# Kernel tuning notes

Measured on AMD Instinct MI355X. Metric: run time of the kernel, lower is better.

Reference implementation:

```python
import jax, jax.numpy as jnp
import numpy as np

N = 8192          # total nodes (bipartite: first half left, second half right)
E = 65536         # raw edges
D = 256           # emb_dim
H = 8             # heads
HD = D // H       # head_dim = 32
EAD = 2           # edge_attr_dim


def _init(k, shape, fan_in):
    return (jax.random.normal(k, shape, jnp.float32) / np.sqrt(fan_in)).astype(jnp.float32)


def setup_inputs() -> dict:
    key = jax.random.key(0)
    ks = jax.random.split(key, 16)
    x = jax.random.normal(ks[0], (N, D), jnp.float32)
    src = jax.random.randint(ks[1], (E,), 0, N // 2, jnp.int32)
    dst = jax.random.randint(ks[2], (E,), N // 2, N, jnp.int32)
    edge_index = jnp.stack([src, dst])                       # [2, E]
    edge_attr = jax.random.uniform(ks[3], (E, EAD), jnp.float32)
    query_mask = jax.random.randint(ks[4], (E,), 0, 2, jnp.int32).astype(bool)
    return {
        "x": x,
        "edge_index": edge_index,
        "edge_attr": edge_attr,
        "query_mask": query_mask,
        "start_right": N // 2,
        "W_kqv": _init(ks[5], (D, 3 * D), D), "b_kqv": jnp.zeros((3 * D,), jnp.float32),
        "W_edge": _init(ks[6], (EAD, D), EAD), "b_edge": jnp.zeros((D,), jnp.float32),
        "W_att1": _init(ks[7], (3 * HD, HD), 3 * HD), "b_att1": jnp.zeros((HD,), jnp.float32),
        "W_att2": _init(ks[8], (HD, 1), HD), "b_att2": jnp.zeros((1,), jnp.float32),
        "W_out": _init(ks[9], (D, D), D), "b_out": jnp.zeros((D,), jnp.float32),
        "bn_gamma": jnp.ones((D,), jnp.float32), "bn_beta": jnp.zeros((D,), jnp.float32),
    }


def _build_graph(edge_index, query_mask, n):
    """Replicates MetaGNN.forward edge preprocessing (static, int-only)."""
    ei = np.asarray(edge_index)
    qm = np.asarray(query_mask).astype(bool)
    sup = np.where(~qm)[0]                                   # support edges
    # cat([edge_index[:, support], edge_index.flip(0)], dim=1)
    src = np.concatenate([ei[0, sup], ei[1]])
    dst = np.concatenate([ei[1, sup], ei[0]])
    attr_idx = np.concatenate([sup, np.arange(ei.shape[1])])
    # remove_self_loops
    keep = src != dst
    src, dst, attr_idx = src[keep], dst[keep], attr_idx[keep]
    # add_self_loops with fill_value [0, 0]
    loops = np.arange(n)
    src = np.concatenate([src, loops])
    dst = np.concatenate([dst, loops])
    return jnp.asarray(src), jnp.asarray(dst), jnp.asarray(attr_idx)


def _layer(x, src, dst, ea, W_kqv, b_kqv, W_edge, b_edge, W_att1, b_att1,
           W_att2, b_att2, W_out, b_out, bn_gamma, bn_beta):
    n = x.shape[0]
    kqv = x @ W_kqv + b_kqv                                  # [N, 3D]
    q = kqv[dst, :D].reshape(-1, H, HD)                      # x_i (target)
    k = kqv[src, D:2 * D].reshape(-1, H, HD) / np.sqrt(HD)   # x_j (source)
    v = kqv[src, 2 * D:].reshape(-1, H, HD)
    ef = jax.nn.relu((ea @ W_edge + b_edge).reshape(-1, H, HD))
    feat = jnp.concatenate([k, q, ef], axis=-1)              # [E, H, 3*HD]
    hdn = jax.nn.relu(jnp.einsum('ehf,fd->ehd', feat, W_att1) + b_att1)
    logits = (jnp.einsum('ehd,do->eho', hdn, W_att2) + b_att2)[..., 0]  # [E, H]
    # scatter-softmax over destination node segments
    m = jax.ops.segment_max(logits, dst, num_segments=n)
    a = jnp.exp(logits - m[dst])
    s = jax.ops.segment_sum(a, dst, num_segments=n)
    alpha = a / (s[dst] + 1e-16)                             # [E, H]
    msg = (alpha[..., None] * v).reshape(-1, D) @ W_out + b_out
    out = jax.ops.segment_sum(msg, dst, num_segments=n) + x  # aggr='add' + residual
    # BatchNorm1d (training-mode batch statistics, eps=1e-5)
    mu = out.mean(axis=0)
    var = out.var(axis=0)
    return (out - mu) / jnp.sqrt(var + 1e-5) * bn_gamma + bn_beta


def reference(x, edge_index, edge_attr, query_mask, start_right,
              W_kqv, b_kqv, W_edge, b_edge, W_att1, b_att1, W_att2, b_att2,
              W_out, b_out, bn_gamma, bn_beta):
    n = x.shape[0]
    src, dst, attr_idx = _build_graph(edge_index, query_mask, n)
    ea = jnp.concatenate(
        [edge_attr[attr_idx], jnp.zeros((n, edge_attr.shape[1]), edge_attr.dtype)], axis=0)
    return _layer(x, src, dst, ea, W_kqv, b_kqv, W_edge, b_edge,
                  W_att1, b_att1, W_att2, b_att2, W_out, b_out, bn_gamma, bn_beta)
```

## Files before the change

### kernel.cpp

```cpp
#include <hip/hip_runtime.h>

#define N_NODES 8192
#define E_RAW   65536
#define NSLOT   (2*E_RAW + N_NODES)
#define DEGCAP  48
#define L_ITER  4

typedef __attribute__((ext_vector_type(8)))  short bf16x8;
typedef __attribute__((ext_vector_type(4)))  short bf16x4;
typedef __attribute__((ext_vector_type(4)))  float f32x4;
typedef __attribute__((ext_vector_type(16))) float f32x16;
typedef unsigned short u16;

__device__ __forceinline__ u16 f2b(float f) {
  unsigned u = __float_as_uint(f);
  u = (u + 0x7FFFu + ((u >> 16) & 1u)) >> 16;
  return (u16)u;
}
__device__ __forceinline__ float b2f(u16 b) {
  return __uint_as_float(((unsigned)b) << 16);
}

__global__ __launch_bounds__(256) void setup_k(
    const float* __restrict__ x, u16* __restrict__ xb,
    const float* __restrict__ W_kqv, const float* __restrict__ b_kqv,
    const float* __restrict__ W_att1, const float* __restrict__ b_att1,
    const float* __restrict__ W_edge, const float* __restrict__ b_edge,
    const float* __restrict__ W_out,
    u16* __restrict__ BcatT, float* __restrict__ biascat,
    u16* __restrict__ wa1t, u16* __restrict__ WoutT, float* __restrict__ beW,
    const int* __restrict__ ei, const int* __restrict__ qm,
    int* __restrict__ cnt, int* __restrict__ csr)
{
  __shared__ float tile[64][65];
  const float inv_sqrt_hd = 0.17677669529663687f;
  int bx = blockIdx.x, t = threadIdx.x;

  if (bx < 2048) {
    int i = bx * 256 + t;
    float4 v = ((const float4*)x)[i];
    ushort4 o;
    o.x = f2b(v.x); o.y = f2b(v.y); o.z = f2b(v.z); o.w = f2b(v.w);
    ((ushort4*)xb)[i] = o;
    return;
  }
  if (bx < 2836) {
    int c = bx - 2048;
    int i = t;
    if (c < 768) {
      float v;
      if (c < 256) {
        int h = c >> 5, d2 = c & 31;
        float s = 0.f;
        #pragma unroll
        for (int j = 0; j < 32; ++j)
          s += W_kqv[i*768 + 256 + h*32 + j] * W_att1[j*32 + d2];
        v = s * inv_sqrt_hd;
      } else if (c < 512) {
        int c2 = c - 256; int h = c2 >> 5, d2 = c2 & 31;
        float s = 0.f;
        #pragma unroll
        for (int j = 0; j < 32; ++j)
          s += W_kqv[i*768 + h*32 + j] * W_att1[(32+j)*32 + d2];
        v = s;
      } else {
        v = W_kqv[i*768 + c];
      }
      BcatT[(size_t)c * 256 + i] = f2b(v);
      if (i == 0) {
        float bv;
        if (c < 256) {
          int h = c >> 5, d2 = c & 31;
          float s = 0.f;
          for (int j = 0; j < 32; ++j)
            s += b_kqv[256 + h*32 + j] * W_att1[j*32 + d2];
          bv = s * inv_sqrt_hd;
        } else if (c < 512) {
          int c2 = c - 256; int h = c2 >> 5, d2 = c2 & 31;
          float s = 0.f;
          for (int j = 0; j < 32; ++j)
            s += b_kqv[h*32 + j] * W_att1[(32+j)*32 + d2];
          bv = s + b_att1[c2 & 31];
        } else {
          bv = b_kqv[c];
        }
        biascat[c] = bv;
      }
    } else if (c < 772) {
      int idx = (c - 768) * 256 + i;
      int d2 = idx >> 5, j = idx & 31;
      wa1t[idx] = f2b(W_att1[(64 + j) * 32 + d2]);
    } else {
      int b = c - 772;
      int r0 = (b >> 2) * 64, c0 = (b & 3) * 64;
      for (int idx = i; idx < 4096; idx += 256) {
        int r = idx >> 6, cc = idx & 63;
        tile[r][cc] = W_out[(size_t)(r0 + r) * 256 + c0 + cc];
      }
      __syncthreads();
      for (int idx = i; idx < 4096; idx += 256) {
        int cc = idx >> 6, r = idx & 63;
        WoutT[(size_t)(c0 + cc) * 256 + r0 + r] = f2b(tile[r][cc]);
      }
    }
    return;
  }
  if (bx == 2836) {
    int h = t >> 5, d2 = t & 31;
    float s = 0.f;
    #pragma unroll
    for (int f = 0; f < 32; ++f)
      s += fmaxf(b_edge[h*32 + f], 0.f) * W_att1[(64 + f)*32 + d2];
    beW[h*32 + d2] = s;
    return;
  }
  int slot = (bx - 2837) * 256 + t;
  if (slot >= NSLOT) return;
  int src, dst;
  if (slot < E_RAW) {
    if (qm[slot] != 0) return;
    src = ei[slot]; dst = ei[E_RAW + slot];
  } else if (slot < 2*E_RAW) {
    int e = slot - E_RAW;
    src = ei[E_RAW + e]; dst = ei[e];
  } else {
    int n = slot - 2*E_RAW;
    src = n; dst = n;
  }
  int pos = atomicAdd(&cnt[dst], 1);
  if (pos < DEGCAP) csr[dst*DEGCAP + pos] = (slot << 13) | src;
}

__global__ __launch_bounds__(256) void gemm_nf_k(const u16* __restrict__ xb,
                                                 const u16* __restrict__ BcatT,
                                                 const float* __restrict__ biascat,
                                                 u16* __restrict__ nodeF) {
  int t = threadIdx.x, lane = t & 63, wid = t >> 6;
  int r0 = (blockIdx.y * 4 + wid) * 32;
  int c0 = blockIdx.x * 32;
  int lr = lane & 15, lk = (lane >> 4) * 8;
  f32x4 acc00 = {0.f,0.f,0.f,0.f}, acc01 = {0.f,0.f,0.f,0.f};
  f32x4 acc10 = {0.f,0.f,0.f,0.f}, acc11 = {0.f,0.f,0.f,0.f};
  for (int k0 = 0; k0 < 256; k0 += 32) {
    bf16x8 a0 = *(const bf16x8*)&xb[(size_t)(r0 + lr) * 256 + k0 + lk];
    bf16x8 a1 = *(const bf16x8*)&xb[(size_t)(r0 + 16 + lr) * 256 + k0 + lk];
    bf16x8 b0 = *(const bf16x8*)&BcatT[(size_t)(c0 + lr) * 256 + k0 + lk];
    bf16x8 b1 = *(const bf16x8*)&BcatT[(size_t)(c0 + 16 + lr) * 256 + k0 + lk];
    acc00 = __builtin_amdgcn_mfma_f32_16x16x32_bf16(a0, b0, acc00, 0, 0, 0);
    acc01 = __builtin_amdgcn_mfma_f32_16x16x32_bf16(a0, b1, acc01, 0, 0, 0);
    acc10 = __builtin_amdgcn_mfma_f32_16x16x32_bf16(a1, b0, acc10, 0, 0, 0);
    acc11 = __builtin_amdgcn_mfma_f32_16x16x32_bf16(a1, b1, acc11, 0, 0, 0);
  }
  float bias0 = biascat[c0 + lr];
  float bias1 = biascat[c0 + 16 + lr];
  int rbase = r0 + (lane >> 4) * 4;
  #pragma unroll
  for (int r = 0; r < 4; ++r) {
    nodeF[(size_t)(rbase + r) * 768 + c0 + lr]           = f2b(acc00[r] + bias0);
    nodeF[(size_t)(rbase + r) * 768 + c0 + 16 + lr]      = f2b(acc01[r] + bias1);
    nodeF[(size_t)(rbase + 16 + r) * 768 + c0 + lr]      = f2b(acc10[r] + bias0);
    nodeF[(size_t)(rbase + 16 + r) * 768 + c0 + 16 + lr] = f2b(acc11[r] + bias1);
  }
}

__global__ __launch_bounds__(256) void logits_k(
    const int* __restrict__ ei, const int* __restrict__ qm,
    const float* __restrict__ eattr, const u16* __restrict__ nf,
    const u16* __restrict__ wa1t,
    const float* __restrict__ W_edge, const float* __restrict__ b_edge,
    const float* __restrict__ W_att2, const float* __restrict__ beW,
    float* __restrict__ lgd)
{
  __shared__ __align__(16) u16 kqls[4][16][8][40];

  int bx = blockIdx.x, t = threadIdx.x, lane = t & 63, wid = t >> 6;
  int col = lane & 31;
  int e = col >> 3, h = col & 7, hi = lane >> 5;

  float w2r[16];
  #pragma unroll
  for (int r = 0; r < 16; ++r)
    w2r[r] = W_att2[(r & 3) + 8*(r >> 2) + 4*hi];

  if (bx < 1024) {
    float ce0[16], ce1[16], cbe[16];
    #pragma unroll
    for (int i = 0; i < 8; ++i) {
      int fA = hi*8 + i, fB = 16 + hi*8 + i;
      ce0[i]   = W_edge[h*32 + fA];       ce0[8+i] = W_edge[h*32 + fB];
      ce1[i]   = W_edge[256 + h*32 + fA]; ce1[8+i] = W_edge[256 + h*32 + fB];
      cbe[i]   = b_edge[h*32 + fA];       cbe[8+i] = b_edge[h*32 + fB];
    }
    bf16x8 af0 = *(const bf16x8*)&wa1t[(lane & 31)*32 + hi*8];
    bf16x8 af1 = *(const bf16x8*)&wa1t[(lane & 31)*32 + 16 + hi*8];

    for (int it = 0; it < L_ITER; ++it) {
      int er0 = ((bx * L_ITER + it) * 4 + wid) * 4;
      int er = er0 + e;
      int eqm = qm[er];
      float2 ea = *(const float2*)&eattr[2*er];

      #pragma unroll
      for (int m = 0; m < 8; ++m) {
        int flat = m*64 + lane;
        int ri = flat >> 5, chunk = flat & 31;
        int ee = ri & 3, ty = ri >> 2;
        int erow = er0 + ee;
        int node = (ty & 1) ? ei[E_RAW + erow] : ei[erow];
        int koff = (ty >> 1) ? 256 : 0;
        bf16x8 v = *(const bf16x8*)&nf[(size_t)node*768 + koff + chunk*8];
        *(bf16x8*)&kqls[wid][ri][chunk >> 2][(chunk & 3)*8] = v;
      }

      bf16x8 bf0, bf1;
      #pragma unroll
      for (int i = 0; i < 8; ++i) {
        float v0 = fmaf(ea.x, ce0[i],   fmaf(ea.y, ce1[i],   cbe[i]));
        float v1 = fmaf(ea.x, ce0[8+i], fmaf(ea.y, ce1[8+i], cbe[8+i]));
        bf0[i] = (short)f2b(fmaxf(v0, 0.f));
        bf1[i] = (short)f2b(fmaxf(v1, 0.f));
      }
      f32x16 acc = {};
      acc = __builtin_amdgcn_mfma_f32_32x32x16_bf16(af0, bf0, acc, 0, 0, 0);
      acc = __builtin_amdgcn_mfma_f32_32x32x16_bf16(af1, bf1, acc, 0, 0, 0);

      __builtin_amdgcn_wave_barrier();

      float lg0 = 0.f, lg1 = 0.f;
      #pragma unroll
      for (int q = 0; q < 4; ++q) {
        int off = q*8 + 4*hi;
        bf16x4 k0 = *(const bf16x4*)&kqls[wid][e][h][off];
        bf16x4 q0 = *(const bf16x4*)&kqls[wid][12 + e][h][off];
        bf16x4 k1 = *(const bf16x4*)&kqls[wid][4 + e][h][off];
        bf16x4 q1 = *(const bf16x4*)&kqls[wid][8 + e][h][off];
        #pragma unroll
        for (int j = 0; j < 4; ++j) {
          int r = q*4 + j;
          float efw = acc[r];
          float p0 = efw + b2f((u16)k0[j]) + b2f((u16)q0[j]);
          float p1 = efw + b2f((u16)k1[j]) + b2f((u16)q1[j]);
          lg0 = fmaf(fmaxf(p0, 0.f), w2r[r], lg0);
          lg1 = fmaf(fmaxf(p1, 0.f), w2r[r], lg1);
        }
      }
      lg0 += __shfl_xor(lg0, 32);
      lg1 += __shfl_xor(lg1, 32);
      if (hi == 0) {
        if (eqm == 0) lgd[(size_t)er*8 + h] = lg0;
        lgd[(size_t)(E_RAW + er)*8 + h] = lg1;
      }
      __builtin_amdgcn_wave_barrier();
    }
  } else {
    float bew[16];
    #pragma unroll
    for (int r = 0; r < 16; ++r)
      bew[r] = beW[h*32 + (r & 3) + 8*(r >> 2) + 4*hi];

    for (int it = 0; it < L_ITER; ++it) {
      int n0 = (((bx - 1024) * L_ITER + it) * 4 + wid) * 4;
      int nn = n0 + e;
      #pragma unroll
      for (int m = 0; m < 4; ++m) {
        int flat = m*64 + lane;
        int ri = flat >> 5, chunk = flat & 31;
        int ee = ri & 3, ty = ri >> 2;
        int node = n0 + ee;
        bf16x8 v = *(const bf16x8*)&nf[(size_t)node*768 + (ty ? 256 : 0) + chunk*8];
        *(bf16x8*)&kqls[wid][ri][chunk >> 2][(chunk & 3)*8] = v;
      }
      __builtin_amdgcn_wave_barrier();
      float lg0 = 0.f;
      #pragma unroll
      for (int q = 0; q < 4; ++q) {
        int off = q*8 + 4*hi;
        bf16x4 k0 = *(const bf16x4*)&kqls[wid][e][h][off];
        bf16x4 q0 = *(const bf16x4*)&kqls[wid][4 + e][h][off];
        #pragma unroll
        for (int j = 0; j < 4; ++j) {
          int r = q*4 + j;
          float p = bew[r] + b2f((u16)k0[j]) + b2f((u16)q0[j]);
          lg0 = fmaf(fmaxf(p, 0.f), w2r[r], lg0);
        }
      }
      lg0 += __shfl_xor(lg0, 32);
      if (hi == 0) lgd[(size_t)(2*E_RAW + nn)*8 + h] = lg0;
      __builtin_amdgcn_wave_barrier();
    }
  }
}

__global__ __launch_bounds__(256) void aggr_k(const int* __restrict__ cnt,
                                              const int* __restrict__ csr,
                                              const float* __restrict__ lgd,
                                              const u16* __restrict__ nf,
                                              u16* __restrict__ aggb) {
  int t = threadIdx.x, lane = t & 63, wid = t >> 6;
  int n = blockIdx.x * 4 + wid;
  int deg = cnt[n]; if (deg > DEGCAP) deg = DEGCAP;

  float m = -3.4e38f, s = 0.f;
  for (int i = lane >> 3; i < deg; i += 8) {
    int pk = csr[n*DEGCAP + i];
    float val = lgd[(size_t)((unsigned)pk >> 13)*8 + (lane & 7)];
    float mn = fmaxf(m, val);
    s = s * __expf(m - mn) + __expf(val - mn);
    m = mn;
  }
  #pragma unroll
  for (int msk = 8; msk <= 32; msk <<= 1) {
    float mo = __shfl_xor(m, msk), so = __shfl_xor(s, msk);
    float mn = fmaxf(m, mo);
    s = s * __expf(m - mn) + so * __expf(mo - mn);
    m = mn;
  }
  float sinv = 1.f / (s + 1e-16f);
  int head = lane >> 3;
  float mh = __shfl(m, head);
  float sh = __shfl(sinv, head);

  float ac0 = 0.f, ac1 = 0.f, ac2 = 0.f, ac3 = 0.f;
  const u16* vb = nf + 512 + lane * 4;
  #pragma unroll 2
  for (int i = 0; i < deg; ++i) {
    int pk = csr[n*DEGCAP + i];
    int slot = (unsigned)pk >> 13, srcv = pk & 8191;
    float a = __expf(lgd[(size_t)slot*8 + head] - mh) * sh;
    bf16x4 v = *(const bf16x4*)&vb[(size_t)srcv * 768];
    ac0 = fmaf(a, b2f((u16)v[0]), ac0);
    ac1 = fmaf(a, b2f((u16)v[1]), ac1);
    ac2 = fmaf(a, b2f((u16)v[2]), ac2);
    ac3 = fmaf(a, b2f((u16)v[3]), ac3);
  }
  ushort4 o; o.x = f2b(ac0); o.y = f2b(ac1); o.z = f2b(ac2); o.w = f2b(ac3);
  *(ushort4*)&aggb[(size_t)n * 256 + lane * 4] = o;
}

__global__ __launch_bounds__(256) void gemmout_k(const u16* __restrict__ aggb,
                                                 const u16* __restrict__ WoutT,
                                                 const float* __restrict__ x,
                                                 const int* __restrict__ cnt,
                                                 const float* __restrict__ b_out,
                                                 float* __restrict__ out,
                                                 float* __restrict__ bnsum,
                                                 float* __restrict__ bnsq) {
  int t = threadIdx.x, lane = t & 63, wid = t >> 6;
  int r0 = (blockIdx.y * 4 + wid) * 32;
  int c0 = blockIdx.x * 32;
  int lr = lane & 15, lk = (lane >> 4) * 8;
  f32x4 acc00 = {0.f,0.f,0.f,0.f}, acc01 = {0.f,0.f,0.f,0.f};
  f32x4 acc10 = {0.f,0.f,0.f,0.f}, acc11 = {0.f,0.f,0.f,0.f};
  for (int k0 = 0; k0 < 256; k0 += 32) {
    bf16x8 a0 = *(const bf16x8*)&aggb[(size_t)(r0 + lr) * 256 + k0 + lk];
    bf16x8 a1 = *(const bf16x8*)&aggb[(size_t)(r0 + 16 + lr) * 256 + k0 + lk];
    bf16x8 b0 = *(const bf16x8*)&WoutT[(size_t)(c0 + lr) * 256 + k0 + lk];
    bf16x8 b1 = *(const bf16x8*)&WoutT[(size_t)(c0 + 16 + lr) * 256 + k0 + lk];
    acc00 = __builtin_amdgcn_mfma_f32_16x16x32_bf16(a0, b0, acc00, 0, 0, 0);
    acc01 = __builtin_amdgcn_mfma_f32_16x16x32_bf16(a0, b1, acc01, 0, 0, 0);
    acc10 = __builtin_amdgcn_mfma_f32_16x16x32_bf16(a1, b0, acc10, 0, 0, 0);
    acc11 = __builtin_amdgcn_mfma_f32_16x16x32_bf16(a1, b1, acc11, 0, 0, 0);
  }
  int colA = c0 + lr, colB = c0 + 16 + lr;
  float bA = b_out[colA], bB = b_out[colB];
  int rbase = r0 + (lane >> 4) * 4;
  float sA = 0.f, qA = 0.f, sB = 0.f, qB = 0.f;
  #pragma unroll
  for (int r = 0; r < 4; ++r) {
    int rowA = rbase + r, rowB = rbase + 16 + r;
    float degA = (float)cnt[rowA], degB = (float)cnt[rowB];
    float v00 = acc00[r] + x[(size_t)rowA * 256 + colA] + degA * bA;
    float v01 = acc01[r] + x[(size_t)rowA * 256 + colB] + degA * bB;
    float v10 = acc10[r] + x[(size_t)rowB * 256 + colA] + degB * bA;
    float v11 = acc11[r] + x[(size_t)rowB * 256 + colB] + degB * bB;
    out[(size_t)rowA * 256 + colA] = v00;
    out[(size_t)rowA * 256 + colB] = v01;
    out[(size_t)rowB * 256 + colA] = v10;
    out[(size_t)rowB * 256 + colB] = v11;
    sA += v00 + v10; qA += v00*v00 + v10*v10;
    sB += v01 + v11; qB += v01*v01 + v11*v11;
  }
  #pragma unroll
  for (int msk = 16; msk <= 32; msk <<= 1) {
    sA += __shfl_xor(sA, msk); qA += __shfl_xor(qA, msk);
    sB += __shfl_xor(sB, msk); qB += __shfl_xor(qB, msk);
  }
  if (lane < 16) {
    atomicAdd(&bnsum[colA], sA); atomicAdd(&bnsq[colA], qA);
    atomicAdd(&bnsum[colB], sB); atomicAdd(&bnsq[colB], qB);
  }
}

__global__ __launch_bounds__(256) void bnapply_k(float* __restrict__ out,
                                                 const float* __restrict__ bnsum,
                                                 const float* __restrict__ bnsq,
                                                 const float* __restrict__ gamma,
                                                 const float* __restrict__ beta) {
  int t = threadIdx.x;
  int c4 = t & 63;
  int r = blockIdx.x * 4 + (t >> 6);
  float4 s4 = ((const float4*)bnsum)[c4];
  float4 q4 = ((const float4*)bnsq)[c4];
  float4 g4 = ((const float4*)gamma)[c4];
  float4 b4 = ((const float4*)beta)[c4];
  float4 v = ((const float4*)out)[(size_t)r * 64 + c4];
  #pragma unroll
  for (int j = 0; j < 4; ++j) {
    float mu = (&s4.x)[j] * (1.f / 8192.f);
    float var = (&q4.x)[j] * (1.f / 8192.f) - mu*mu;
    float inv = rsqrtf(var + 1e-5f);
    (&v.x)[j] = ((&v.x)[j] - mu) * inv * (&g4.x)[j] + (&b4.x)[j];
  }
  ((float4*)out)[(size_t)r * 64 + c4] = v;
}

extern "C" void kernel_launch(void* const* d_in, const int* in_sizes, int n_in,
                              void* d_out, int out_size, void* d_ws, size_t ws_size,
                              hipStream_t stream) {
  (void)in_sizes; (void)n_in; (void)out_size; (void)ws_size;
  const float* x      = (const float*)d_in[0];
  const int*   ei     = (const int*)d_in[1];
  const float* eattr  = (const float*)d_in[2];
  const int*   qm     = (const int*)d_in[3];
  const float* W_kqv  = (const float*)d_in[5];
  const float* b_kqv  = (const float*)d_in[6];
  const float* W_edge = (const float*)d_in[7];
  const float* b_edge = (const float*)d_in[8];
  const float* W_att1 = (const float*)d_in[9];
  const float* b_att1 = (const float*)d_in[10];
  const float* W_att2 = (const float*)d_in[11];
  const float* W_out  = (const float*)d_in[13];
  const float* b_out  = (const float*)d_in[14];
  const float* gamma  = (const float*)d_in[15];
  const float* beta   = (const float*)d_in[16];
  float* out = (float*)d_out;

  char* w = (char*)d_ws;
  u16*    xb      = (u16*)w;     w += (size_t)N_NODES*256*2;
  u16*    BcatT   = (u16*)w;     w += (size_t)768*256*2;
  u16*    wa1t    = (u16*)w;     w += 1024*2;
  u16*    WoutT   = (u16*)w;     w += (size_t)256*256*2;
  u16*    nodeFb  = (u16*)w;     w += (size_t)N_NODES*768*2;
  float*  biascat = (float*)w;   w += 768*4;
  float*  beW     = (float*)w;   w += 256*4;
  u16*    aggb    = (u16*)w;     w += (size_t)N_NODES*256*2;
  int*    cnt     = (int*)w;     w += N_NODES*4;
  float*  bnsum   = (float*)w;   w += 256*4;
  float*  bnsq    = (float*)w;   w += 256*4;
  int*    csr     = (int*)w;     w += (size_t)N_NODES*DEGCAP*4;
  float*  lgd     = (float*)w;   w += (size_t)NSLOT*8*4;

  hipMemsetAsync(cnt, 0, (size_t)(N_NODES + 512) * sizeof(int), stream);

  setup_k<<<2837 + (NSLOT + 255)/256, 256, 0, stream>>>(
      x, xb, W_kqv, b_kqv, W_att1, b_att1, W_edge, b_edge, W_out,
      BcatT, biascat, wa1t, WoutT, beW, ei, qm, cnt, csr);

  gemm_nf_k<<<dim3(768/32, N_NODES/128), 256, 0, stream>>>(xb, BcatT, biascat, nodeFb);

  logits_k<<<1024 + 128, 256, 0, stream>>>(ei, qm, eattr, nodeFb, wa1t,
                                           W_edge, b_edge, W_att2, beW, lgd);

  aggr_k<<<N_NODES/4, 256, 0, stream>>>(cnt, csr, lgd, nodeFb, aggb);

  gemmout_k<<<dim3(256/32, N_NODES/128), 256, 0, stream>>>(
      aggb, WoutT, x, cnt, b_out, out, bnsum, bnsq);

  bnapply_k<<<N_NODES/4, 256, 0, stream>>>(out, bnsum, bnsq, gamma, beta);
}
```

Baseline: 109.9 us.

## Replace memset with in-kernel zeroing and fuse CSR scatter into widened node GEMM

Removes the hipMemsetAsync by zeroing the counter/BN-sum region (2176 int4 = 8704 ints) inside setup_k's extra blocks. The edge-to-CSR scatter moves out of setup_k into the node-feature GEMM kernel, which now tiles 128x64 per block with 8 accumulators instead of 128x32. This cuts one launch and the memset, and lets the scatter atomics overlap the GEMM. The cost is higher register use in the GEMM blocks and a mixed-role grid.

```diff
diff --git a/kernel.cpp b/kernel.cpp
--- a/kernel.cpp
+++ b/kernel.cpp
@@ -29,8 +29,7 @@
     const float* __restrict__ W_out,
     u16* __restrict__ BcatT, float* __restrict__ biascat,
     u16* __restrict__ wa1t, u16* __restrict__ WoutT, float* __restrict__ beW,
-    const int* __restrict__ ei, const int* __restrict__ qm,
-    int* __restrict__ cnt, int* __restrict__ csr)
+    int4* __restrict__ zbase)
 {
   __shared__ float tile[64][65];
   const float inv_sqrt_hd = 0.17677669529663687f;
@@ -114,7 +113,53 @@
     beW[h*32 + d2] = s;
     return;
   }
-  int slot = (bx - 2837) * 256 + t;
+  int i = (bx - 2837) * 256 + t;
+  if (i < 2176) zbase[i] = make_int4(0, 0, 0, 0);
+}
+
+__global__ __launch_bounds__(256) void gemm_scatter_k(
+    const u16* __restrict__ xb, const u16* __restrict__ BcatT,
+    const float* __restrict__ biascat, u16* __restrict__ nodeF,
+    const int* __restrict__ ei, const int* __restrict__ qm,
+    int* __restrict__ cnt, int* __restrict__ csr)
+{
+  int bx = blockIdx.x, t = threadIdx.x;
+  if (bx < 768) {
+    int lane = t & 63, wid = t >> 6;
+    int cb = bx % 12, rb = bx / 12;
+    int r0 = rb * 128 + wid * 32;
+    int c0 = cb * 64;
+    int lr = lane & 15, lk = (lane >> 4) * 8;
+    f32x4 acc0[4] = {}, acc1[4] = {};
+    for (int k0 = 0; k0 < 256; k0 += 32) {
+      bf16x8 a0 = *(const bf16x8*)&xb[(size_t)(r0 + lr) * 256 + k0 + lk];
+      bf16x8 a1 = *(const bf16x8*)&xb[(size_t)(r0 + 16 + lr) * 256 + k0 + lk];
+      bf16x8 b0 = *(const bf16x8*)&BcatT[(size_t)(c0 + lr) * 256 + k0 + lk];
+      bf16x8 b1 = *(const bf16x8*)&BcatT[(size_t)(c0 + 16 + lr) * 256 + k0 + lk];
+      bf16x8 b2 = *(const bf16x8*)&BcatT[(size_t)(c0 + 32 + lr) * 256 + k0 + lk];
+      bf16x8 b3 = *(const bf16x8*)&BcatT[(size_t)(c0 + 48 + lr) * 256 + k0 + lk];
+      acc0[0] = __builtin_amdgcn_mfma_f32_16x16x32_bf16(a0, b0, acc0[0], 0, 0, 0);
+      acc0[1] = __builtin_amdgcn_mfma_f32_16x16x32_bf16(a0, b1, acc0[1], 0, 0, 0);
+      acc0[2] = __builtin_amdgcn_mfma_f32_16x16x32_bf16(a0, b2, acc0[2], 0, 0, 0);
+      acc0[3] = __builtin_amdgcn_mfma_f32_16x16x32_bf16(a0, b3, acc0[3], 0, 0, 0);
+      acc1[0] = __builtin_amdgcn_mfma_f32_16x16x32_bf16(a1, b0, acc1[0], 0, 0, 0);
+      acc1[1] = __builtin_amdgcn_mfma_f32_16x16x32_bf16(a1, b1, acc1[1], 0, 0, 0);
+      acc1[2] = __builtin_amdgcn_mfma_f32_16x16x32_bf16(a1, b2, acc1[2], 0, 0, 0);
+      acc1[3] = __builtin_amdgcn_mfma_f32_16x16x32_bf16(a1, b3, acc1[3], 0, 0, 0);
+    }
+    int rbase = r0 + (lane >> 4) * 4;
+    #pragma unroll
+    for (int cc = 0; cc < 4; ++cc) {
+      float bias = biascat[c0 + cc*16 + lr];
+      #pragma unroll
+      for (int r = 0; r < 4; ++r) {
+        nodeF[(size_t)(rbase + r) * 768 + c0 + cc*16 + lr]      = f2b(acc0[cc][r] + bias);
+        nodeF[(size_t)(rbase + 16 + r) * 768 + c0 + cc*16 + lr] = f2b(acc1[cc][r] + bias);
+      }
+    }
+    return;
+  }
+  int slot = (bx - 768) * 256 + t;
   if (slot >= NSLOT) return;
   int src, dst;
   if (slot < E_RAW) {
@@ -129,38 +174,6 @@
   }
   int pos = atomicAdd(&cnt[dst], 1);
   if (pos < DEGCAP) csr[dst*DEGCAP + pos] = (slot << 13) | src;
-}
-
-__global__ __launch_bounds__(256) void gemm_nf_k(const u16* __restrict__ xb,
-                                                 const u16* __restrict__ BcatT,
-                                                 const float* __restrict__ biascat,
-                                                 u16* __restrict__ nodeF) {
-  int t = threadIdx.x, lane = t & 63, wid = t >> 6;
-  int r0 = (blockIdx.y * 4 + wid) * 32;
-  int c0 = blockIdx.x * 32;
-  int lr = lane & 15, lk = (lane >> 4) * 8;
-  f32x4 acc00 = {0.f,0.f,0.f,0.f}, acc01 = {0.f,0.f,0.f,0.f};
-  f32x4 acc10 = {0.f,0.f,0.f,0.f}, acc11 = {0.f,0.f,0.f,0.f};
-  for (int k0 = 0; k0 < 256; k0 += 32) {
-    bf16x8 a0 = *(const bf16x8*)&xb[(size_t)(r0 + lr) * 256 + k0 + lk];
-    bf16x8 a1 = *(const bf16x8*)&xb[(size_t)(r0 + 16 + lr) * 256 + k0 + lk];
-    bf16x8 b0 = *(const bf16x8*)&BcatT[(size_t)(c0 + lr) * 256 + k0 + lk];
-    bf16x8 b1 = *(const bf16x8*)&BcatT[(size_t)(c0 + 16 + lr) * 256 + k0 + lk];
-    acc00 = __builtin_amdgcn_mfma_f32_16x16x32_bf16(a0, b0, acc00, 0, 0, 0);
-    acc01 = __builtin_amdgcn_mfma_f32_16x16x32_bf16(a0, b1, acc01, 0, 0, 0);
-    acc10 = __builtin_amdgcn_mfma_f32_16x16x32_bf16(a1, b0, acc10, 0, 0, 0);
-    acc11 = __builtin_amdgcn_mfma_f32_16x16x32_bf16(a1, b1, acc11, 0, 0, 0);
-  }
-  float bias0 = biascat[c0 + lr];
-  float bias1 = biascat[c0 + 16 + lr];
-  int rbase = r0 + (lane >> 4) * 4;
-  #pragma unroll
-  for (int r = 0; r < 4; ++r) {
-    nodeF[(size_t)(rbase + r) * 768 + c0 + lr]           = f2b(acc00[r] + bias0);
-    nodeF[(size_t)(rbase + r) * 768 + c0 + 16 + lr]      = f2b(acc01[r] + bias1);
-    nodeF[(size_t)(rbase + 16 + r) * 768 + c0 + lr]      = f2b(acc10[r] + bias0);
-    nodeF[(size_t)(rbase + 16 + r) * 768 + c0 + 16 + lr] = f2b(acc11[r] + bias1);
-  }
 }
 
 __global__ __launch_bounds__(256) void logits_k(
@@ -450,13 +463,12 @@
   int*    csr     = (int*)w;     w += (size_t)N_NODES*DEGCAP*4;
   float*  lgd     = (float*)w;   w += (size_t)NSLOT*8*4;
 
-  hipMemsetAsync(cnt, 0, (size_t)(N_NODES + 512) * sizeof(int), stream);
-
-  setup_k<<<2837 + (NSLOT + 255)/256, 256, 0, stream>>>(
+  setup_k<<<2846, 256, 0, stream>>>(
       x, xb, W_kqv, b_kqv, W_att1, b_att1, W_edge, b_edge, W_out,
-      BcatT, biascat, wa1t, WoutT, beW, ei, qm, cnt, csr);
-
-  gemm_nf_k<<<dim3(768/32, N_NODES/128), 256, 0, stream>>>(xb, BcatT, biascat, nodeFb);
+      BcatT, biascat, wa1t, WoutT, beW, (int4*)cnt);
+
+  gemm_scatter_k<<<768 + (NSLOT + 255)/256, 256, 0, stream>>>(
+      xb, BcatT, biascat, nodeFb, ei, qm, cnt, csr);
 
   logits_k<<<1024 + 128, 256, 0, stream>>>(ei, qm, eattr, nodeFb, wa1t,
                                            W_edge, b_edge, W_att2, beW, lgd);
```

Measured after the change: 102.0 us. 1.08x faster.
